# Kernel optimization log

Measured on AMD Instinct MI355X. Metric: run time of the kernel, lower is better.

## Reference

```python
import jax, jax.numpy as jnp
import numpy as np

B, S, E = 2, 4096, 512

def setup_inputs() -> dict:
    key = jax.random.key(0)
    kx, kq, kk, kv, ko = jax.random.split(key, 5)
    scale = 1.0 / np.sqrt(E)  # init-style scaling for weights
    return {
        "x": jax.random.normal(kx, (B, S, E), dtype=jnp.float32),
        "Wq": jax.random.normal(kq, (E, E), dtype=jnp.float32) * scale,
        "Wk": jax.random.normal(kk, (E, E), dtype=jnp.float32) * scale,
        "Wv": jax.random.normal(kv, (E, E), dtype=jnp.float32) * scale,
        "Wo": jax.random.normal(ko, (E, E), dtype=jnp.float32) * scale,
        "bo": jnp.zeros((E,), dtype=jnp.float32),
    }

def reference(x, Wq, Wk, Wv, Wo, bo):
    # nn.Linear: y = x @ W.T  (weights stored [out, in])
    q = jnp.einsum("bse,fe->bsf", x, Wq)
    k = jnp.einsum("bse,fe->bsf", x, Wk)
    v = jnp.einsum("bse,fe->bsf", x, Wv)
    inv_scale = 1.0 / jnp.sqrt(jnp.asarray(x.shape[-1], x.dtype))
    scores = jnp.einsum("bqe,bke->bqk", q, k) * inv_scale  # [B,S,S]
    S_len = x.shape[1]
    # torch.triu(ones) keeps j >= i; masked_fill where triu==0 masks j < i
    row = jnp.arange(S_len)[:, None]
    col = jnp.arange(S_len)[None, :]
    keep = col >= row  # [S,S], faithfully anti-causal as in the source
    scores = jnp.where(keep[None, :, :], scores, jnp.asarray(-jnp.inf, scores.dtype))
    attn = jax.nn.softmax(scores, axis=-1)
    # dropout p=0.0 -> identity
    out = jnp.einsum("bqk,bke->bqe", attn, v)
    return jnp.einsum("bse,fe->bsf", out, Wo) + bo
```

## Files before the change

### kernel.cpp

```cpp
#include <hip/hip_runtime.h>
#include <hip/hip_bf16.h>

#define S_LEN 4096
#define E_DIM 512
#define B_DIM 2
#define M_ROWS (B_DIM * S_LEN)

typedef __attribute__((ext_vector_type(8))) short short8;
typedef __attribute__((ext_vector_type(4))) float floatx4;

__device__ __forceinline__ unsigned short f2bf(float f) {
    unsigned u = __float_as_uint(f);
    unsigned r = (u + 0x7fffu + ((u >> 16) & 1u)) >> 16;
    return (unsigned short)r;
}
__device__ __forceinline__ float bf2f(unsigned short u) {
    return __uint_as_float((unsigned)u << 16);
}

__device__ __forceinline__ void async_copy16(unsigned short* lds, const unsigned short* g) {
    auto gp = (const __attribute__((address_space(1))) unsigned int*)g;
    auto lp = (__attribute__((address_space(3))) unsigned int*)lds;
    __builtin_amdgcn_global_load_lds(gp, lp, 16, 0, 0);
}

struct MapArg { unsigned short m[576]; };

__global__ __launch_bounds__(256) void convert_bf16(
    const float* __restrict__ x,  const float* __restrict__ wq,
    const float* __restrict__ wk, const float* __restrict__ wv,
    const float* __restrict__ wo, unsigned short* __restrict__ dstU,
    unsigned short* __restrict__ dstWo)
{
    long i = (long)blockIdx.x * 1024 + (long)threadIdx.x * 4;
    const float* src; long off; unsigned short* dst; long doff;
    if      (i < 4194304) { src = x;  off = i;           dst = dstU;  doff = i; }
    else if (i < 4456448) { src = wq; off = i - 4194304; dst = dstU;  doff = i; }
    else if (i < 4718592) { src = wk; off = i - 4456448; dst = dstU;  doff = i; }
    else if (i < 4980736) { src = wv; off = i - 4718592; dst = dstU;  doff = i; }
    else                  { src = wo; off = i - 4980736; dst = dstWo; doff = i - 4980736; }
    float4 v = *(const float4*)(src + off);
    ushort4 o;
    o.x = f2bf(v.x); o.y = f2bf(v.y); o.z = f2bf(v.z); o.w = f2bf(v.w);
    *(ushort4*)(dst + doff) = o;
}

__device__ __forceinline__ void gemm_core(
    const unsigned short* __restrict__ A, const unsigned short* __restrict__ W,
    void* __restrict__ Cv, const float* __restrict__ bias, int mode,
    int m0, int n0)
{
    __shared__ unsigned short As[128 * 64];
    __shared__ unsigned short Bs[128 * 64];
    const int tid = threadIdx.x;
    const int lane = tid & 63, wave = tid >> 6;
    const int wm = wave >> 1, wn = wave & 1;
    const int q4 = lane >> 4, l16 = lane & 15;
    const int er = l16 & 7;

    floatx4 acc[4][4];
#pragma unroll
    for (int i = 0; i < 4; ++i)
#pragma unroll
        for (int j = 0; j < 4; ++j) acc[i][j] = (floatx4){0.f, 0.f, 0.f, 0.f};

    const int srow = lane >> 3;
    const int scol = ((lane & 7) ^ srow) << 3;

    for (int k0 = 0; k0 < 512; k0 += 64) {
#pragma unroll
        for (int c = 0; c < 4; ++c) {
            const int rbase = c * 32 + wave * 8;
            async_copy16(&As[rbase * 64],
                         A + (size_t)(m0 + rbase + srow) * 512 + k0 + scol);
            async_copy16(&Bs[rbase * 64],
                         W + (size_t)(n0 + rbase + srow) * 512 + k0 + scol);
        }
        __syncthreads();
        short8 af[4][2], bfr[4][2];
        const int c0 = (q4 ^ er) * 8;
#pragma unroll
        for (int i = 0; i < 4; ++i) {
            const int ra = (wm * 64 + i * 16 + l16) * 64;
            const int rb = (wn * 64 + i * 16 + l16) * 64;
            af[i][0]  = *(const short8*)&As[ra + c0];
            af[i][1]  = *(const short8*)&As[ra + (c0 ^ 32)];
            bfr[i][0] = *(const short8*)&Bs[rb + c0];
            bfr[i][1] = *(const short8*)&Bs[rb + (c0 ^ 32)];
        }
#pragma unroll
        for (int h = 0; h < 2; ++h)
#pragma unroll
            for (int i = 0; i < 4; ++i)
#pragma unroll
                for (int j = 0; j < 4; ++j)
                    acc[i][j] = __builtin_amdgcn_mfma_f32_16x16x32_bf16(
                        af[i][h], bfr[j][h], acc[i][j], 0, 0, 0);
        __syncthreads();
    }

    if (mode == 0) {
        unsigned short* C = (unsigned short*)Cv;
#pragma unroll
        for (int i = 0; i < 4; ++i) {
            int rowb = m0 + wm * 64 + i * 16 + q4 * 4;
#pragma unroll
            for (int j = 0; j < 4; ++j) {
                int col = n0 + wn * 64 + j * 16 + l16;
#pragma unroll
                for (int rg = 0; rg < 4; ++rg)
                    C[(size_t)(rowb + rg) * 512 + col] = f2bf(acc[i][j][rg]);
            }
        }
    } else if (mode == 1) {
        unsigned short* C = (unsigned short*)Cv;
#pragma unroll
        for (int i = 0; i < 4; ++i) {
            int grow = m0 + wm * 64 + i * 16 + q4 * 4;
            int b = grow >> 12, s = grow & 4095;
#pragma unroll
            for (int j = 0; j < 4; ++j) {
                int e = n0 + wn * 64 + j * 16 + l16;
                ushort4 pk;
                pk.x = f2bf(acc[i][j][0]); pk.y = f2bf(acc[i][j][1]);
                pk.z = f2bf(acc[i][j][2]); pk.w = f2bf(acc[i][j][3]);
                *(ushort4*)(C + (size_t)b * 512 * 4096 + (size_t)e * 4096 + s) = pk;
            }
        }
    } else {
        float* C = (float*)Cv;
#pragma unroll
        for (int i = 0; i < 4; ++i) {
            int rowb = m0 + wm * 64 + i * 16 + q4 * 4;
#pragma unroll
            for (int j = 0; j < 4; ++j) {
                int col = n0 + wn * 64 + j * 16 + l16;
                float bv = bias[col];
#pragma unroll
                for (int rg = 0; rg < 4; ++rg)
                    C[(size_t)(rowb + rg) * 512 + col] = acc[i][j][rg] + bv;
            }
        }
    }
}

__global__ __launch_bounds__(256) void gemm_qkv(
    const unsigned short* __restrict__ xb,
    const unsigned short* __restrict__ Wqb, const unsigned short* __restrict__ Wkb,
    const unsigned short* __restrict__ Wvb,
    unsigned short* __restrict__ Qb, unsigned short* __restrict__ Kb,
    unsigned short* __restrict__ Vtb)
{
    const int z = blockIdx.z;
    const unsigned short* W = (z == 0) ? Wqb : (z == 1) ? Wkb : Wvb;
    unsigned short* C = (z == 0) ? Qb : (z == 1) ? Kb : Vtb;
    gemm_core(xb, W, C, nullptr, (z == 2) ? 1 : 0, blockIdx.y * 128, blockIdx.x * 128);
}

__global__ __launch_bounds__(256) void gemm_out(
    const unsigned short* __restrict__ AOb, const unsigned short* __restrict__ Wob,
    const float* __restrict__ bo, float* __restrict__ out)
{
    gemm_core(AOb, Wob, out, bo, 2, blockIdx.y * 128, blockIdx.x * 128);
}

__global__ __launch_bounds__(512, 2) void flash_mfma(
    const unsigned short* __restrict__ Qg, const unsigned short* __restrict__ Kg,
    const unsigned short* __restrict__ Vt,
    unsigned short* __restrict__ Oh, float* __restrict__ Lb, MapArg map)
{
    const int enc = map.m[blockIdx.x];
    const int tile = enc & 63, ch = (enc >> 6) & 7, bb = enc >> 9;
    const int i0 = tile * 64;
    const int lo0 = 512 * ch, hi = lo0 + 512;
    const int lo = (i0 > lo0) ? i0 : lo0;
    const int lo_al = lo & ~127;
    const int nsteps = (hi - lo_al) >> 7;

    const int tid = threadIdx.x;
    const int lane = tid & 63, w = tid >> 6;
    const int q4 = lane >> 4, l16 = lane & 15;
    const int e = l16 & 7;
    const float scale = 0.044194173824159216f;
    const float MREF = 4.0f;

    __shared__ unsigned short Qs[64 * 512];
    __shared__ unsigned short Plds[2][64][136];
    __shared__ float Lred[8][64];

    const size_t rowbase = (size_t)bb * S_LEN;
    const size_t vbase   = (size_t)bb * (size_t)512 * 4096;

#pragma unroll
    for (int rr = 0; rr < 8; ++rr) {
        const int row = w * 8 + rr;
        const unsigned short* src = Qg + (rowbase + i0 + row) * 512
                                    + ((lane ^ (row & 7)) << 3);
        async_copy16(&Qs[row * 512], src);
    }

    floatx4 oacc[4][4];
#pragma unroll
    for (int mg = 0; mg < 4; ++mg)
#pragma unroll
        for (int nc = 0; nc < 4; ++nc) oacc[mg][nc] = (floatx4){0.f, 0.f, 0.f, 0.f};
    float l_acc[4] = {0.f, 0.f, 0.f, 0.f};

    const unsigned short* qb0 = &Qs[l16 * 512 + ((q4 ^ e) << 3)];
    const unsigned short* qb1 = &Qs[l16 * 512 + (((q4 + 4) ^ e) << 3)];
    const unsigned short* kpbase = Kg + (rowbase + 16 * w + l16) * 512 + (q4 << 3);

    __syncthreads();

    for (int t = 0; t < nsteps; ++t) {
        const int j0 = lo_al + t * 128;
        const int buf = t & 1;

        short8 kf[16];
        const unsigned short* kp = kpbase + (size_t)j0 * 512;
#pragma unroll
        for (int ks = 0; ks < 16; ++ks)
            kf[ks] = *(const short8*)(kp + ks * 32);

        short8 vf[4][4];
#pragma unroll
        for (int nc = 0; nc < 4; ++nc) {
            const unsigned short* vpn = Vt + vbase
                + (size_t)(w * 64 + nc * 16 + l16) * 4096 + j0 + (q4 << 3);
#pragma unroll
            for (int kslot = 0; kslot < 4; ++kslot)
                vf[nc][kslot] = *(const short8*)(vpn + kslot * 32);
        }

        floatx4 sfe[4], sfo[4];
#pragma unroll
        for (int mg = 0; mg < 4; ++mg) {
            sfe[mg] = (floatx4){0.f, 0.f, 0.f, 0.f};
            sfo[mg] = (floatx4){0.f, 0.f, 0.f, 0.f};
        }
        __builtin_amdgcn_s_setprio(1);
#pragma unroll
        for (int ks = 0; ks < 16; ++ks) {
            const unsigned short* qb = (ks & 1) ? qb1 : qb0;
#pragma unroll
            for (int mg = 0; mg < 4; ++mg) {
                short8 a = *(const short8*)(qb + mg * 8192 + (ks >> 1) * 64);
                if (ks & 1)
                    sfo[mg] = __builtin_amdgcn_mfma_f32_16x16x32_bf16(kf[ks], a, sfo[mg], 0, 0, 0);
                else
                    sfe[mg] = __builtin_amdgcn_mfma_f32_16x16x32_bf16(kf[ks], a, sfe[mg], 0, 0, 0);
            }
        }
        __builtin_amdgcn_s_setprio(0);

        const int kb = j0 + 16 * w + (q4 << 2);
        const bool full = (j0 >= i0 + 64);
#pragma unroll
        for (int mg = 0; mg < 4; ++mg) {
            const int row = i0 + mg * 16 + l16;
            float s0 = sfe[mg][0] + sfo[mg][0];
            float s1 = sfe[mg][1] + sfo[mg][1];
            float s2 = sfe[mg][2] + sfo[mg][2];
            float s3 = sfe[mg][3] + sfo[mg][3];
            float p0 = __expf(s0 * scale - MREF);
            float p1 = __expf(s1 * scale - MREF);
            float p2 = __expf(s2 * scale - MREF);
            float p3 = __expf(s3 * scale - MREF);
            if (!full) {
                p0 = (kb + 0 >= row) ? p0 : 0.f;
                p1 = (kb + 1 >= row) ? p1 : 0.f;
                p2 = (kb + 2 >= row) ? p2 : 0.f;
                p3 = (kb + 3 >= row) ? p3 : 0.f;
            }
            l_acc[mg] += p0 + p1 + p2 + p3;
            ushort4 pk;
            pk.x = f2bf(p0); pk.y = f2bf(p1); pk.z = f2bf(p2); pk.w = f2bf(p3);
            *(ushort4*)&Plds[buf][mg * 16 + l16][16 * w + (q4 << 2)] = pk;
        }
        __syncthreads();

        __builtin_amdgcn_s_setprio(1);
#pragma unroll
        for (int kslot = 0; kslot < 4; ++kslot) {
#pragma unroll
            for (int mg = 0; mg < 4; ++mg) {
                short8 ap = *(const short8*)&Plds[buf][mg * 16 + l16][kslot * 32 + (q4 << 3)];
#pragma unroll
                for (int nc = 0; nc < 4; ++nc)
                    oacc[mg][nc] = __builtin_amdgcn_mfma_f32_16x16x32_bf16(
                        ap, vf[nc][kslot], oacc[mg][nc], 0, 0, 0);
            }
        }
        __builtin_amdgcn_s_setprio(0);
    }

#pragma unroll
    for (int mg = 0; mg < 4; ++mg) {
        float v = l_acc[mg];
        v += __shfl_xor(v, 16, 64);
        v += __shfl_xor(v, 32, 64);
        if (q4 == 0) Lred[w][mg * 16 + l16] = v;
    }
    __syncthreads();

    const int slot = 8 * ch * (ch + 1) + bb * 8 * (ch + 1) + tile;
    if (tid < 64) {
        float sum = 0.f;
#pragma unroll
        for (int ww = 0; ww < 8; ++ww) sum += Lred[ww][tid];
        Lb[(size_t)slot * 64 + tid] = sum;
    }

    unsigned short* Op = Oh + (size_t)slot * 64 * 512;
#pragma unroll
    for (int mg = 0; mg < 4; ++mg)
#pragma unroll
        for (int nc = 0; nc < 4; ++nc)
#pragma unroll
            for (int rg = 0; rg < 4; ++rg)
                Op[(size_t)(mg * 16 + q4 * 4 + rg) * 512 + w * 64 + nc * 16 + l16]
                    = f2bf(oacc[mg][nc][rg]);
}

__global__ __launch_bounds__(256) void flash_merge(
    const unsigned short* __restrict__ Oh, const float* __restrict__ Lb,
    unsigned short* __restrict__ AO)
{
    const int row = blockIdx.x * 4 + (threadIdx.x >> 6);
    const int c0 = (threadIdx.x & 63) * 8;
    const int bb = row >> 12, i = row & 4095;
    const int t = i >> 6, ri = i & 63;
    const int chmin = i >> 9;
    float lsum = 0.f;
    float v[8] = {0.f, 0.f, 0.f, 0.f, 0.f, 0.f, 0.f, 0.f};
    for (int ch = chmin; ch < 8; ++ch) {
        int slot = 8 * ch * (ch + 1) + bb * 8 * (ch + 1) + t;
        lsum += Lb[(size_t)slot * 64 + ri];
        short8 p = *(const short8*)(Oh + (size_t)slot * 64 * 512
                                    + (size_t)ri * 512 + c0);
#pragma unroll
        for (int k = 0; k < 8; ++k) v[k] += bf2f((unsigned short)p[k]);
    }
    float inv = 1.f / lsum;
    short8 o;
#pragma unroll
    for (int k = 0; k < 8; ++k) o[k] = (short)f2bf(v[k] * inv);
    *(short8*)(AO + (size_t)row * 512 + c0) = o;
}

static MapArg build_map() {
    MapArg mp{};
    for (int x = 0; x < 8; ++x) {
        const int bb = x >> 2;
        const int chs[2] = {7 - (x & 3), x & 3};
        int enc[72], st[72], n = 0;
        for (int ci = 0; ci < 2; ++ci) {
            const int ch = chs[ci];
            for (int t = 0; t < 8 * (ch + 1); ++t) {
                int i0 = t * 64, lo0 = 512 * ch, hi = lo0 + 512;
                int lo = (i0 > lo0) ? i0 : lo0;
                int lo_al = lo & ~127;
                enc[n] = t | (ch << 6) | (bb << 9);
                st[n] = (hi - lo_al) >> 7;
                ++n;
            }
        }
        for (int i = 1; i < n; ++i) {
            int ev = enc[i], sv = st[i], j = i - 1;
            while (j >= 0 && st[j] < sv) { st[j + 1] = st[j]; enc[j + 1] = enc[j]; --j; }
            st[j + 1] = sv; enc[j + 1] = ev;
        }
        for (int j = 0; j < n; ++j) mp.m[x + 8 * j] = (unsigned short)enc[j];
    }
    return mp;
}

extern "C" void kernel_launch(void* const* d_in, const int* in_sizes, int n_in,
                              void* d_out, int out_size, void* d_ws, size_t ws_size,
                              hipStream_t stream) {
    (void)in_sizes; (void)n_in; (void)out_size; (void)ws_size;
    const float* x  = (const float*)d_in[0];
    const float* Wq = (const float*)d_in[1];
    const float* Wk = (const float*)d_in[2];
    const float* Wv = (const float*)d_in[3];
    const float* Wo = (const float*)d_in[4];
    const float* bo = (const float*)d_in[5];
    float* out = (float*)d_out;

    unsigned short* ws  = (unsigned short*)d_ws;
    unsigned short* Wob = ws;
    unsigned short* QAb = ws + 262144;
    unsigned short* Kb  = QAb + 4194304;
    unsigned short* Vtb = Kb + 4194304;
    unsigned short* U   = Vtb + 4194304;
    unsigned short* xb  = U;
    unsigned short* Wqb = U + 4194304;
    unsigned short* Wkb = Wqb + 262144;
    unsigned short* Wvb = Wkb + 262144;
    unsigned short* Ohb = U;
    float* Lbf = (float*)(U + 18874368);

    static const MapArg mp = build_map();

    convert_bf16<<<5120, 256, 0, stream>>>(x, Wq, Wk, Wv, Wo, U, Wob);

    gemm_qkv<<<dim3(4, 64, 3), 256, 0, stream>>>(xb, Wqb, Wkb, Wvb, QAb, Kb, Vtb);

    flash_mfma<<<576, 512, 0, stream>>>(QAb, Kb, Vtb, Ohb, Lbf, mp);

    flash_merge<<<2048, 256, 0, stream>>>(Ohb, Lbf, QAb);

    gemm_out<<<dim3(4, 64), 256, 0, stream>>>(QAb, Wob, bo, out);
}
```

Measured before the change: 226.3 us.

## Widen flash attention key tile to 256 and stream V fragments per k-slot

Doubles the key block processed per iteration from 128 to 256, so each wave computes two 16-key score tiles and the loop runs half as many times with half as many barriers. V fragments are no longer loaded up front for the whole tile but double-buffered in registers one k-slot ahead inside the PV loop. This cuts per-iteration sync and loop overhead and keeps register pressure manageable despite the larger K fragment set. In exchange it wastes more masked work near the diagonal because of the coarser 256 alignment, and it enlarges the P LDS buffer, which may reduce occupancy.

```diff
diff --git a/kernel.cpp b/kernel.cpp
--- a/kernel.cpp
+++ b/kernel.cpp
@@ -174,8 +174,8 @@
     const int i0 = tile * 64;
     const int lo0 = 512 * ch, hi = lo0 + 512;
     const int lo = (i0 > lo0) ? i0 : lo0;
-    const int lo_al = lo & ~127;
-    const int nsteps = (hi - lo_al) >> 7;
+    const int lo_al = lo & ~255;
+    const int nsteps = (hi - lo_al) >> 8;
 
     const int tid = threadIdx.x;
     const int lane = tid & 63, w = tid >> 6;
@@ -185,7 +185,7 @@
     const float MREF = 4.0f;
 
     __shared__ unsigned short Qs[64 * 512];
-    __shared__ unsigned short Plds[2][64][136];
+    __shared__ unsigned short Plds[2][64][264];
     __shared__ float Lred[8][64];
 
     const size_t rowbase = (size_t)bb * S_LEN;
@@ -208,35 +208,31 @@
 
     const unsigned short* qb0 = &Qs[l16 * 512 + ((q4 ^ e) << 3)];
     const unsigned short* qb1 = &Qs[l16 * 512 + (((q4 + 4) ^ e) << 3)];
-    const unsigned short* kpbase = Kg + (rowbase + 16 * w + l16) * 512 + (q4 << 3);
+    const unsigned short* kpbaseA = Kg + (rowbase + 32 * w + l16) * 512 + (q4 << 3);
+    const unsigned short* kpbaseB = kpbaseA + (size_t)16 * 512;
+    const unsigned short* vpbase = Vt + vbase + (size_t)(w * 64 + l16) * 4096 + (q4 << 3);
 
     __syncthreads();
 
     for (int t = 0; t < nsteps; ++t) {
-        const int j0 = lo_al + t * 128;
+        const int j0 = lo_al + t * 256;
         const int buf = t & 1;
 
-        short8 kf[16];
-        const unsigned short* kp = kpbase + (size_t)j0 * 512;
-#pragma unroll
-        for (int ks = 0; ks < 16; ++ks)
-            kf[ks] = *(const short8*)(kp + ks * 32);
-
-        short8 vf[4][4];
-#pragma unroll
-        for (int nc = 0; nc < 4; ++nc) {
-            const unsigned short* vpn = Vt + vbase
-                + (size_t)(w * 64 + nc * 16 + l16) * 4096 + j0 + (q4 << 3);
-#pragma unroll
-            for (int kslot = 0; kslot < 4; ++kslot)
-                vf[nc][kslot] = *(const short8*)(vpn + kslot * 32);
-        }
-
-        floatx4 sfe[4], sfo[4];
+        short8 kfA[16], kfB[16];
+        {
+            const unsigned short* kpA = kpbaseA + (size_t)j0 * 512;
+            const unsigned short* kpB = kpbaseB + (size_t)j0 * 512;
+#pragma unroll
+            for (int ks = 0; ks < 16; ++ks) kfA[ks] = *(const short8*)(kpA + ks * 32);
+#pragma unroll
+            for (int ks = 0; ks < 16; ++ks) kfB[ks] = *(const short8*)(kpB + ks * 32);
+        }
+
+        floatx4 sfA[4], sfB[4];
 #pragma unroll
         for (int mg = 0; mg < 4; ++mg) {
-            sfe[mg] = (floatx4){0.f, 0.f, 0.f, 0.f};
-            sfo[mg] = (floatx4){0.f, 0.f, 0.f, 0.f};
+            sfA[mg] = (floatx4){0.f, 0.f, 0.f, 0.f};
+            sfB[mg] = (floatx4){0.f, 0.f, 0.f, 0.f};
         }
         __builtin_amdgcn_s_setprio(1);
 #pragma unroll
@@ -245,51 +241,71 @@
 #pragma unroll
             for (int mg = 0; mg < 4; ++mg) {
                 short8 a = *(const short8*)(qb + mg * 8192 + (ks >> 1) * 64);
-                if (ks & 1)
-                    sfo[mg] = __builtin_amdgcn_mfma_f32_16x16x32_bf16(kf[ks], a, sfo[mg], 0, 0, 0);
-                else
-                    sfe[mg] = __builtin_amdgcn_mfma_f32_16x16x32_bf16(kf[ks], a, sfe[mg], 0, 0, 0);
+                sfA[mg] = __builtin_amdgcn_mfma_f32_16x16x32_bf16(kfA[ks], a, sfA[mg], 0, 0, 0);
+                sfB[mg] = __builtin_amdgcn_mfma_f32_16x16x32_bf16(kfB[ks], a, sfB[mg], 0, 0, 0);
             }
         }
         __builtin_amdgcn_s_setprio(0);
 
-        const int kb = j0 + 16 * w + (q4 << 2);
+        short8 vc[4], vn[4];
+#pragma unroll
+        for (int nc = 0; nc < 4; ++nc)
+            vc[nc] = *(const short8*)(vpbase + (size_t)(nc * 16) * 4096 + j0);
+#pragma unroll
+        for (int nc = 0; nc < 4; ++nc)
+            vn[nc] = *(const short8*)(vpbase + (size_t)(nc * 16) * 4096 + j0 + 32);
+
+        const int kbA = j0 + 32 * w + (q4 << 2);
         const bool full = (j0 >= i0 + 64);
 #pragma unroll
         for (int mg = 0; mg < 4; ++mg) {
             const int row = i0 + mg * 16 + l16;
-            float s0 = sfe[mg][0] + sfo[mg][0];
-            float s1 = sfe[mg][1] + sfo[mg][1];
-            float s2 = sfe[mg][2] + sfo[mg][2];
-            float s3 = sfe[mg][3] + sfo[mg][3];
-            float p0 = __expf(s0 * scale - MREF);
-            float p1 = __expf(s1 * scale - MREF);
-            float p2 = __expf(s2 * scale - MREF);
-            float p3 = __expf(s3 * scale - MREF);
+            float pA0 = __expf(sfA[mg][0] * scale - MREF);
+            float pA1 = __expf(sfA[mg][1] * scale - MREF);
+            float pA2 = __expf(sfA[mg][2] * scale - MREF);
+            float pA3 = __expf(sfA[mg][3] * scale - MREF);
+            float pB0 = __expf(sfB[mg][0] * scale - MREF);
+            float pB1 = __expf(sfB[mg][1] * scale - MREF);
+            float pB2 = __expf(sfB[mg][2] * scale - MREF);
+            float pB3 = __expf(sfB[mg][3] * scale - MREF);
             if (!full) {
-                p0 = (kb + 0 >= row) ? p0 : 0.f;
-                p1 = (kb + 1 >= row) ? p1 : 0.f;
-                p2 = (kb + 2 >= row) ? p2 : 0.f;
-                p3 = (kb + 3 >= row) ? p3 : 0.f;
-            }
-            l_acc[mg] += p0 + p1 + p2 + p3;
-            ushort4 pk;
-            pk.x = f2bf(p0); pk.y = f2bf(p1); pk.z = f2bf(p2); pk.w = f2bf(p3);
-            *(ushort4*)&Plds[buf][mg * 16 + l16][16 * w + (q4 << 2)] = pk;
+                pA0 = (kbA + 0 >= row) ? pA0 : 0.f;
+                pA1 = (kbA + 1 >= row) ? pA1 : 0.f;
+                pA2 = (kbA + 2 >= row) ? pA2 : 0.f;
+                pA3 = (kbA + 3 >= row) ? pA3 : 0.f;
+                pB0 = (kbA + 16 >= row) ? pB0 : 0.f;
+                pB1 = (kbA + 17 >= row) ? pB1 : 0.f;
+                pB2 = (kbA + 18 >= row) ? pB2 : 0.f;
+                pB3 = (kbA + 19 >= row) ? pB3 : 0.f;
+            }
+            l_acc[mg] += pA0 + pA1 + pA2 + pA3 + pB0 + pB1 + pB2 + pB3;
+            ushort4 pkA, pkB;
+            pkA.x = f2bf(pA0); pkA.y = f2bf(pA1); pkA.z = f2bf(pA2); pkA.w = f2bf(pA3);
+            pkB.x = f2bf(pB0); pkB.y = f2bf(pB1); pkB.z = f2bf(pB2); pkB.w = f2bf(pB3);
+            *(ushort4*)&Plds[buf][mg * 16 + l16][32 * w + (q4 << 2)] = pkA;
+            *(ushort4*)&Plds[buf][mg * 16 + l16][32 * w + 16 + (q4 << 2)] = pkB;
         }
         __syncthreads();
 
         __builtin_amdgcn_s_setprio(1);
 #pragma unroll
-        for (int kslot = 0; kslot < 4; ++kslot) {
+        for (int kslot = 0; kslot < 8; ++kslot) {
+            if (kslot < 7) {
+#pragma unroll
+                for (int nc = 0; nc < 4; ++nc)
+                    vn[nc] = *(const short8*)(vpbase + (size_t)(nc * 16) * 4096
+                                              + j0 + (kslot + 1) * 32);
+            }
 #pragma unroll
             for (int mg = 0; mg < 4; ++mg) {
                 short8 ap = *(const short8*)&Plds[buf][mg * 16 + l16][kslot * 32 + (q4 << 3)];
 #pragma unroll
                 for (int nc = 0; nc < 4; ++nc)
                     oacc[mg][nc] = __builtin_amdgcn_mfma_f32_16x16x32_bf16(
-                        ap, vf[nc][kslot], oacc[mg][nc], 0, 0, 0);
-            }
+                        ap, vc[nc], oacc[mg][nc], 0, 0, 0);
+            }
+#pragma unroll
+            for (int nc = 0; nc < 4; ++nc) vc[nc] = vn[nc];
         }
         __builtin_amdgcn_s_setprio(0);
     }
@@ -359,9 +375,9 @@
             for (int t = 0; t < 8 * (ch + 1); ++t) {
                 int i0 = t * 64, lo0 = 512 * ch, hi = lo0 + 512;
                 int lo = (i0 > lo0) ? i0 : lo0;
-                int lo_al = lo & ~127;
+                int lo_al = lo & ~255;
                 enc[n] = t | (ch << 6) | (bb << 9);
-                st[n] = (hi - lo_al) >> 7;
+                st[n] = (hi - lo_al) >> 8;
                 ++n;
             }
         }
```

Result: slower. 231.7 us (+2.4%).
